# Performance work log

Measured on AMD Instinct MI355X. Metric: run time of the kernel, lower is better.

## Reference

```python
import jax, jax.numpy as jnp
import numpy as np

V, D, DI, S, B, NI = 32000, 1024, 768, 512, 8, 197
EPS = 1e-5

def _ln(x, g, b):
    m = jnp.mean(x, axis=-1, keepdims=True)
    v = jnp.var(x, axis=-1, keepdims=True)
    return (x - m) * jax.lax.rsqrt(v + EPS) * g + b

def _pos_enc(seq_len, d):
    pos = np.arange(seq_len)[:, None].astype(np.float32)
    i = np.arange(0, d, 2).astype(np.float32)
    ang = pos / np.power(10000.0, i / d)
    pe = np.zeros((seq_len, d), dtype=np.float32)
    pe[:, 0::2] = np.sin(ang)
    pe[:, 1::2] = np.cos(ang)
    return jnp.asarray(pe)

def setup_inputs() -> dict:
    key = jax.random.key(0)
    ks = jax.random.split(key, 24)
    def rn(k, shape, scale=0.02):
        return jax.random.normal(k, shape, dtype=jnp.float32) * scale
    return {
        'tokens': jax.random.randint(ks[0], (B, S), 0, V),
        'img_emb': jax.random.normal(ks[1], (B, NI, DI), dtype=jnp.float32),
        'emb_table': rn(ks[2], (V, D), 1.0),
        'Wq1': rn(ks[3], (D, D)), 'bq1': jnp.zeros((D,), jnp.float32),
        'Wk1': rn(ks[4], (D, D)), 'bk1': jnp.zeros((D,), jnp.float32),
        'Wv1': rn(ks[5], (D, D)), 'bv1': jnp.zeros((D,), jnp.float32),
        'g1': jnp.ones((D,), jnp.float32), 'b1': jnp.zeros((D,), jnp.float32),
        'Wq2': rn(ks[6], (D, D)), 'bq2': jnp.zeros((D,), jnp.float32),
        'Wk2': rn(ks[7], (DI, D)), 'bk2': jnp.zeros((D,), jnp.float32),
        'Wv2': rn(ks[8], (DI, D)), 'bv2': jnp.zeros((D,), jnp.float32),
        'g2': jnp.ones((D,), jnp.float32), 'b2': jnp.zeros((D,), jnp.float32),
        'Wp': rn(ks[9], (D, V)), 'bp': jnp.zeros((V,), jnp.float32),
    }

def _forward(tokens, img_emb, emb_table, Wq1, bq1, Wk1, bk1, Wv1, bv1, g1, b1,
             Wq2, bq2, Wk2, bk2, Wv2, bv2, g2, b2, Wp, bp):
    scale = 1.0 / jnp.sqrt(jnp.float32(D))
    x = emb_table[tokens] + _pos_enc(S, D)[None]  # [B,S,D]
    # masked (causal) self-attention
    Q = x @ Wq1 + bq1
    K = x @ Wk1 + bk1
    Vv = x @ Wv1 + bv1
    attn = jnp.einsum('bqd,bkd->bqk', Q, K) * scale
    causal = jnp.tril(jnp.ones((S, S), dtype=bool))
    attn = jnp.where(causal[None], attn, -jnp.inf)
    A = jax.nn.softmax(attn, axis=-1)
    x = _ln(A @ Vv + x, g1, b1)
    # cross-attention over image tokens
    Q2 = x @ Wq2 + bq2
    K2 = img_emb @ Wk2 + bk2
    V2 = img_emb @ Wv2 + bv2
    A2 = jax.nn.softmax(jnp.einsum('bqd,bkd->bqk', Q2, K2) * scale, axis=-1)
    x = _ln(A2 @ V2 + x, g2, b2)
    # vocab projection (note: Decoder.forward never calls self.ff)
    return x @ Wp + bp  # [B,S,V]

def reference(tokens, img_emb, emb_table, Wq1, bq1, Wk1, bk1, Wv1, bv1, g1, b1,
              Wq2, bq2, Wk2, bk2, Wv2, bv2, g2, b2, Wp, bp):
    return _forward(tokens, img_emb, emb_table, Wq1, bq1, Wk1, bk1, Wv1, bv1, g1, b1,
                    Wq2, bq2, Wk2, bk2, Wv2, bv2, g2, b2, Wp, bp)
```

## Files before the change

kernel.cpp:

```cpp
#include <hip/hip_runtime.h>
#include <hip/hip_bf16.h>


#define DEV __device__ __forceinline__

typedef __bf16 bf16x8 __attribute__((ext_vector_type(8)));
typedef float f32x4 __attribute__((ext_vector_type(4)));
typedef unsigned int u32;
typedef __hip_bfloat16 bf16;

DEV void llds16(const void* g, void* l) {
  __builtin_amdgcn_global_load_lds((const __attribute__((address_space(1))) u32*)g,
                                   (__attribute__((address_space(3))) u32*)l, 16, 0, 0);
}

DEV float wredsum(float v){
#pragma unroll
  for (int o = 32; o; o >>= 1) v += __shfl_xor(v, o, 64);
  return v;
}
DEV float wredmax(float v){
#pragma unroll
  for (int o = 32; o; o >>= 1) v = fmaxf(v, __shfl_xor(v, o, 64));
  return v;
}

DEV void store_out(float* p, float v){ *p = v; }
DEV void store_out(bf16* p, float v){ *p = __float2bfloat16(v); }

template<typename OutT>
__global__ __launch_bounds__(512, 1) void gemm256_kernel(
    const bf16* __restrict__ A, const bf16* __restrict__ Bt, OutT* __restrict__ C,
    const float* __restrict__ bias, int M, int N, int K, int lda, int ldb, int ldc)
{
  __shared__ alignas(16) char lds[131072];
  const int tid  = threadIdx.x;
  const int wave = tid >> 6, lane = tid & 63;
  const int lo = lane & 15, hi = lane >> 4;
  const int hi2 = hi ^ ((lo >> 1) & 3);
  const int wr = wave >> 2, wc = wave & 3;
  const int koff = (((lane & 3) ^ ((lane >> 3) & 3)) << 3);

  const int nbx = M >> 8;
  const int nwg = nbx * (N >> 8);
  int id = blockIdx.x;
  int g = (nwg & 7) ? id : ((id & 7) * (nwg >> 3) + (id >> 3));
  const int row0 = (g % nbx) * 256, col0 = (g / nbx) * 256;
  const int NT = K >> 5;
  const int srow = lane >> 2;

  auto stageA = [&](int t) {
    char* base = lds + (t & 3) * 32768;
    const int kk = (t << 5) + koff;
#pragma unroll
    for (int j = 0; j < 2; j++) {
      const int seg = j * 8 + wave;
      llds16(A + (long)(row0 + seg * 16 + srow) * lda + kk, base + seg * 1024);
    }
  };
  auto stageB = [&](int t) {
    char* base = lds + (t & 3) * 32768 + 16384;
    const int kk = (t << 5) + koff;
#pragma unroll
    for (int j = 0; j < 2; j++) {
      const int seg = j * 8 + wave;
      llds16(Bt + (long)(col0 + seg * 16 + srow) * ldb + kk, base + seg * 1024);
    }
  };

  f32x4 acc[8][4] = {};

  stageA(0); stageB(0);
  stageA(1); stageB(1);
  stageA(2); stageB(2);
  asm volatile("s_waitcnt vmcnt(8)" ::: "memory");
  __builtin_amdgcn_s_barrier();
  asm volatile("" ::: "memory");

  for (int t = 0; t < NT; t++) {
    char* As = lds + (t & 3) * 32768;
    char* Bs = As + 16384;
    bf16x8 af[4], bfv[4];
#pragma unroll
    for (int m = 0; m < 4; m++)
      af[m] = *(const bf16x8*)(As + ((wr * 128 + m * 16 + lo) << 6) + (hi2 << 4));
#pragma unroll
    for (int n = 0; n < 4; n++)
      bfv[n] = *(const bf16x8*)(Bs + ((wc * 64 + n * 16 + lo) << 6) + (hi2 << 4));
    if (t + 3 < NT) stageA(t + 3);
    __builtin_amdgcn_s_setprio(1);
#pragma unroll
    for (int m = 0; m < 4; m++)
#pragma unroll
      for (int n = 0; n < 4; n++)
        acc[m][n] = __builtin_amdgcn_mfma_f32_16x16x32_bf16(af[m], bfv[n], acc[m][n], 0, 0, 0);
    __builtin_amdgcn_s_setprio(0);
    asm volatile("" ::: "memory");
    __builtin_amdgcn_s_barrier();
    asm volatile("" ::: "memory");
#pragma unroll
    for (int m = 0; m < 4; m++)
      af[m] = *(const bf16x8*)(As + ((wr * 128 + (m + 4) * 16 + lo) << 6) + (hi2 << 4));
    if (t + 3 < NT) stageB(t + 3);
    __builtin_amdgcn_s_setprio(1);
#pragma unroll
    for (int m = 0; m < 4; m++)
#pragma unroll
      for (int n = 0; n < 4; n++)
        acc[m + 4][n] = __builtin_amdgcn_mfma_f32_16x16x32_bf16(af[m], bfv[n], acc[m + 4][n], 0, 0, 0);
    __builtin_amdgcn_s_setprio(0);
    if (t < NT - 3)       asm volatile("s_waitcnt vmcnt(8)" ::: "memory");
    else if (t == NT - 3) asm volatile("s_waitcnt vmcnt(4)" ::: "memory");
    else                  asm volatile("s_waitcnt vmcnt(0)" ::: "memory");
    __builtin_amdgcn_s_barrier();
    asm volatile("" ::: "memory");
  }

#pragma unroll
  for (int m = 0; m < 8; m++) {
    const int r = row0 + wr * 128 + m * 16 + hi * 4;
#pragma unroll
    for (int n = 0; n < 4; n++) {
      const int c = col0 + wc * 64 + n * 16 + lo;
      const float bb = bias ? bias[c] : 0.0f;
#pragma unroll
      for (int j = 0; j < 4; j++)
        store_out(&C[(long)(r + j) * ldc + c], acc[m][n][j] + bb);
    }
  }
}

template<typename OutT>
__global__ __launch_bounds__(256) void gemm_bt_kernel(
    const bf16* __restrict__ A, const bf16* __restrict__ Bt, OutT* __restrict__ C,
    const float* __restrict__ bias, int M, int N, int K,
    int lda, int ldb, int ldc, long sA, long sB, long sC)
{
  A  += (long)blockIdx.z * sA;
  Bt += (long)blockIdx.z * sB;
  C  += (long)blockIdx.z * sC;
  __shared__ alignas(16) char lds[32768];
  const int tid = threadIdx.x;
  const int wave = tid >> 6, lane = tid & 63;
  const int lo = lane & 15, hi = lane >> 4;
  const int hi2 = hi ^ ((lo >> 1) & 3);
  const int wr = wave >> 1, wc = wave & 1;
  const int row0 = blockIdx.x * 128, col0 = blockIdx.y * 128;
  const int srow  = lane >> 2;
  const int skoff = (((lane & 3) ^ ((lane >> 3) & 3)) << 3);
  const int NT = K >> 5;

  auto stage = [&](int t) {
    char* base = lds + (t & 1) * 16384;
    const int kk = (t << 5) + skoff;
#pragma unroll
    for (int c = 0; c < 2; ++c) {
      const int seg = c*4 + wave;
      int ra = row0 + seg*16 + srow; ra = ra < M ? ra : M-1;
      llds16(A + (long)ra*lda + kk, base + seg*1024);
      int rb = col0 + seg*16 + srow; rb = rb < N ? rb : N-1;
      llds16(Bt + (long)rb*ldb + kk, base + 8192 + seg*1024);
    }
  };

  f32x4 acc[4][4] = {};

  stage(0);
  asm volatile("s_waitcnt vmcnt(0)" ::: "memory");
  __builtin_amdgcn_s_barrier();
  __builtin_amdgcn_sched_barrier(0);

  for (int t = 0; t < NT; t++) {
    const char* As = lds + (t & 1) * 16384;
    const char* Bs = As + 8192;
    if (t + 1 < NT) stage(t + 1);
    bf16x8 af[4], bfv[4];
#pragma unroll
    for (int m = 0; m < 4; m++)
      af[m] = *(const bf16x8*)(As + ((wr*64 + m*16 + lo) << 6) + (hi2 << 4));
#pragma unroll
    for (int n = 0; n < 4; n++)
      bfv[n] = *(const bf16x8*)(Bs + ((wc*64 + n*16 + lo) << 6) + (hi2 << 4));
    __builtin_amdgcn_s_setprio(1);
#pragma unroll
    for (int m = 0; m < 4; m++)
#pragma unroll
      for (int n = 0; n < 4; n++)
        acc[m][n] = __builtin_amdgcn_mfma_f32_16x16x32_bf16(af[m], bfv[n], acc[m][n], 0, 0, 0);
    __builtin_amdgcn_s_setprio(0);
    __builtin_amdgcn_sched_barrier(0);
    asm volatile("s_waitcnt vmcnt(0)" ::: "memory");
    __builtin_amdgcn_sched_barrier(0);
    __builtin_amdgcn_s_barrier();
    __builtin_amdgcn_sched_barrier(0);
  }

#pragma unroll
  for (int m = 0; m < 4; m++) {
    const int rbase = row0 + wr*64 + m*16 + hi*4;
#pragma unroll
    for (int n = 0; n < 4; n++) {
      const int cc = col0 + wc*64 + n*16 + lo;
      if (cc >= N) continue;
      const float bb = bias ? bias[cc] : 0.0f;
#pragma unroll
      for (int j = 0; j < 4; j++) {
        const int rr = rbase + j;
        if (rr < M) store_out(&C[(long)rr*ldc + cc], acc[m][n][j] + bb);
      }
    }
  }
}

__global__ __launch_bounds__(256) void wprep4_kernel(
    const float* W0, const float* W1, const float* W2, const float* W3,
    bf16* T0, bf16* T1, bf16* T2, bf16* T3, int K, int N)
{
  const int z = blockIdx.z;
  const float* W = z == 0 ? W0 : z == 1 ? W1 : z == 2 ? W2 : W3;
  bf16* T = z == 0 ? T0 : z == 1 ? T1 : z == 2 ? T2 : T3;
  __shared__ bf16 t[32][33];
  const int k0 = blockIdx.x * 32, n0 = blockIdx.y * 32;
  const int tx = threadIdx.x & 31, ty = threadIdx.x >> 5;
#pragma unroll
  for (int i = 0; i < 4; i++)
    t[ty + i*8][tx] = __float2bfloat16(W[(long)(k0 + ty + i*8)*N + n0 + tx]);
  __syncthreads();
#pragma unroll
  for (int i = 0; i < 4; i++)
    T[(long)(n0 + ty + i*8)*K + k0 + tx] = t[tx][ty + i*8];
}

__global__ __launch_bounds__(256) void transpose_pad_kernel(
    const bf16* __restrict__ in, bf16* __restrict__ out,
    int R, int Cc, int inLD, int outLD, long inBatch, long outBatch)
{
  in  += (long)blockIdx.z * inBatch;
  out += (long)blockIdx.z * outBatch;
  __shared__ bf16 t[32][33];
  const int r0 = blockIdx.x * 32, c0 = blockIdx.y * 32;
  const int tx = threadIdx.x & 31, ty = threadIdx.x >> 5;
#pragma unroll
  for (int i = 0; i < 4; i++) {
    const int r = r0 + ty + i*8;
    bf16 v = __float2bfloat16(0.0f);
    if (r < R) v = in[(long)r*inLD + c0 + tx];
    t[ty + i*8][tx] = v;
  }
  __syncthreads();
#pragma unroll
  for (int i = 0; i < 4; i++) {
    const int oc = r0 + tx;
    const int orow = c0 + ty + i*8;
    if (oc < outLD) out[(long)orow*outLD + oc] = t[tx][ty + i*8];
  }
}

__global__ __launch_bounds__(256) void concat_bias_kernel(
    const float* a, const float* b, const float* c, int n1, int n2, int n3, float* out)
{
  const int i = blockIdx.x * 256 + threadIdx.x;
  if (i >= n1 + n2 + n3) return;
  out[i] = i < n1 ? a[i] : (i < n1 + n2 ? b[i - n1] : c[i - n1 - n2]);
}

__global__ __launch_bounds__(256) void embed_kernel(
    const int* __restrict__ tok, const float* __restrict__ tbl,
    float* __restrict__ xf, bf16* __restrict__ xb)
{
  const int row = blockIdx.x;
  const int s = row & 511;
  const float pos = (float)s;
  const float* te = tbl + (long)tok[row] * 1024;
  const int d0 = threadIdx.x * 4;
  float4 v = *(const float4*)(te + d0);
  float o[4] = {v.x, v.y, v.z, v.w};
#pragma unroll
  for (int k = 0; k < 4; k++) {
    const int d = d0 + k;
    const int i2 = d & ~1;
    const float ang = pos * exp2f((float)i2 * -0.0129762816f);
    o[k] += (d & 1) ? __cosf(ang) : __sinf(ang);
  }
  *(float4*)(xf + (long)row*1024 + d0) = make_float4(o[0], o[1], o[2], o[3]);
#pragma unroll
  for (int k = 0; k < 4; k++) xb[(long)row*1024 + d0 + k] = __float2bfloat16(o[k]);
}

__global__ __launch_bounds__(256) void cvt_bf16_kernel(const float* __restrict__ in, bf16* __restrict__ out, long n)
{
  long i = (long)blockIdx.x * blockDim.x + threadIdx.x;
  if (i < n) out[i] = __float2bfloat16(in[i]);
}

__global__ __launch_bounds__(64) void softmax_causal_kernel(
    const float* __restrict__ Sc, bf16* __restrict__ P)
{
  const int row = blockIdx.x;
  const int q = row & 511;
  const float* srow = Sc + (long)row * 512;
  bf16* prow = P + (long)row * 512;
  const int lane = threadIdx.x;
  const float scale = 0.03125f;
  float mx = -1e30f;
  for (int j = lane; j <= q; j += 64) mx = fmaxf(mx, srow[j]);
  mx = wredmax(mx);
  float sum = 0.0f;
  for (int j = lane; j <= q; j += 64) sum += expf((srow[j] - mx) * scale);
  sum = wredsum(sum);
  const float inv = 1.0f / sum;
  for (int j = lane; j < 512; j += 64) {
    float p = (j <= q) ? expf((srow[j] - mx) * scale) * inv : 0.0f;
    prow[j] = __float2bfloat16(p);
  }
}

__global__ __launch_bounds__(64) void softmax_cross_kernel(
    const float* __restrict__ Sc, bf16* __restrict__ P)
{
  const int row = blockIdx.x;
  const float* srow = Sc + (long)row * 224;
  bf16* prow = P + (long)row * 224;
  const int lane = threadIdx.x;
  const float scale = 0.03125f;
  float mx = -1e30f;
  for (int j = lane; j < 197; j += 64) mx = fmaxf(mx, srow[j]);
  mx = wredmax(mx);
  float sum = 0.0f;
  for (int j = lane; j < 197; j += 64) sum += expf((srow[j] - mx) * scale);
  sum = wredsum(sum);
  const float inv = 1.0f / sum;
  for (int j = lane; j < 224; j += 64) {
    float p = (j < 197) ? expf((srow[j] - mx) * scale) * inv : 0.0f;
    prow[j] = __float2bfloat16(p);
  }
}

__global__ __launch_bounds__(256) void add_ln_kernel(
    const float* __restrict__ Acc, const float* __restrict__ Res,
    const float* __restrict__ g, const float* __restrict__ b,
    float* __restrict__ outf, bf16* __restrict__ outb)
{
  const int row = blockIdx.x;
  const float* a = Acc + (long)row * 1024;
  const float* r = Res + (long)row * 1024;
  float vals[4], s = 0.0f, ss = 0.0f;
#pragma unroll
  for (int i = 0; i < 4; i++) {
    const int d = threadIdx.x + i*256;
    const float v = a[d] + r[d];
    vals[i] = v; s += v; ss += v*v;
  }
  s = wredsum(s); ss = wredsum(ss);
  __shared__ float sh[8];
  const int wave = threadIdx.x >> 6, lane = threadIdx.x & 63;
  if (lane == 0) { sh[wave] = s; sh[wave+4] = ss; }
  __syncthreads();
  s  = sh[0] + sh[1] + sh[2] + sh[3];
  ss = sh[4] + sh[5] + sh[6] + sh[7];
  const float mean = s * (1.0f/1024.0f);
  const float var  = ss * (1.0f/1024.0f) - mean*mean;
  const float inv  = rsqrtf(var + 1e-5f);
#pragma unroll
  for (int i = 0; i < 4; i++) {
    const int d = threadIdx.x + i*256;
    const float y = (vals[i] - mean) * inv * g[d] + b[d];
    if (outf) outf[(long)row*1024 + d] = y;
    outb[(long)row*1024 + d] = __float2bfloat16(y);
  }
}

extern "C" void kernel_launch(void* const* d_in, const int* in_sizes, int n_in,
                              void* d_out, int out_size, void* d_ws, size_t ws_size,
                              hipStream_t stream) {
  const int*   tokens = (const int*)  d_in[0];
  const float* img    = (const float*)d_in[1];
  const float* emb    = (const float*)d_in[2];
  const float* Wq1    = (const float*)d_in[3];
  const float* bq1    = (const float*)d_in[4];
  const float* Wk1    = (const float*)d_in[5];
  const float* bk1    = (const float*)d_in[6];
  const float* Wv1    = (const float*)d_in[7];
  const float* bv1    = (const float*)d_in[8];
  const float* g1     = (const float*)d_in[9];
  const float* b1     = (const float*)d_in[10];
  const float* Wq2    = (const float*)d_in[11];
  const float* bq2    = (const float*)d_in[12];
  const float* Wk2    = (const float*)d_in[13];
  const float* bk2    = (const float*)d_in[14];
  const float* Wv2    = (const float*)d_in[15];
  const float* bv2    = (const float*)d_in[16];
  const float* g2     = (const float*)d_in[17];
  const float* b2     = (const float*)d_in[18];
  const float* Wp     = (const float*)d_in[19];
  const float* bp     = (const float*)d_in[20];
  float* out = (float*)d_out;

  const int B = 8, S = 512, D = 1024, DI = 768, NI = 197, NIP = 224, V = 32000;
  const int M = B * S;
  const int MI = B * NI;

  char* ws = (char*)d_ws;
  size_t off = 0;
  auto alloc = [&](size_t bytes) -> char* {
    char* p = ws + off; off += (bytes + 255) & ~(size_t)255; return p;
  };
  bf16* Wq1t = (bf16*)alloc((size_t)D*D*2);
  bf16* Wk1t = (bf16*)alloc((size_t)D*D*2);
  bf16* Wv1t = (bf16*)alloc((size_t)D*D*2);
  bf16* Wq2t = (bf16*)alloc((size_t)D*D*2);
  bf16* Wk2t = (bf16*)alloc((size_t)D*DI*2);
  bf16* Wv2t = (bf16*)alloc((size_t)D*DI*2);
  bf16* Wpt  = (bf16*)alloc((size_t)V*D*2);
  float* bqkv= (float*)alloc((size_t)3*D*4);
  float* bkv2= (float*)alloc((size_t)2*D*4);
  float* xf  = (float*)alloc((size_t)M*D*4);
  bf16*  xb  = (bf16*) alloc((size_t)M*D*2);
  bf16*  imgb= (bf16*) alloc((size_t)MI*DI*2);
  bf16*  QKV = (bf16*) alloc((size_t)M*3*D*2);
  bf16*  Vt  = (bf16*) alloc((size_t)M*D*2);
  float* sc1 = (float*)alloc((size_t)B*S*S*4);
  bf16*  P1  = (bf16*) alloc((size_t)B*S*S*2);
  float* ao1 = (float*)alloc((size_t)M*D*4);
  float* x2f = (float*)alloc((size_t)M*D*4);
  bf16*  x2b = (bf16*) alloc((size_t)M*D*2);
  bf16*  Q2  = (bf16*) alloc((size_t)M*D*2);
  bf16*  KV2 = (bf16*) alloc((size_t)MI*2*D*2);
  bf16*  V2t = (bf16*) alloc((size_t)B*D*NIP*2);
  float* sc2 = (float*)alloc((size_t)B*S*NIP*4);
  bf16*  P2  = (bf16*) alloc((size_t)B*S*NIP*2);
  float* ao2 = (float*)alloc((size_t)M*D*4);
  bf16*  x3b = (bf16*) alloc((size_t)M*D*2);
  (void)ws_size; (void)in_sizes; (void)n_in; (void)out_size;

  wprep4_kernel<<<dim3(D/32,  D/32, 4), 256, 0, stream>>>(Wq1, Wk1, Wv1, Wq2, Wq1t, Wk1t, Wv1t, Wq2t, D, D);
  wprep4_kernel<<<dim3(DI/32, D/32, 2), 256, 0, stream>>>(Wk2, Wv2, nullptr, nullptr, Wk2t, Wv2t, nullptr, nullptr, DI, D);
  wprep4_kernel<<<dim3(D/32,  V/32, 1), 256, 0, stream>>>(Wp, nullptr, nullptr, nullptr, Wpt, nullptr, nullptr, nullptr, D, V);
  concat_bias_kernel<<<(3*D+255)/256, 256, 0, stream>>>(bq1, bk1, bv1, D, D, D, bqkv);
  concat_bias_kernel<<<(2*D+255)/256, 256, 0, stream>>>(bk2, bv2, nullptr, D, D, 0, bkv2);

  embed_kernel<<<M, 256, 0, stream>>>(tokens, emb, xf, xb);
  {
    long n = (long)MI * DI;
    cvt_bf16_kernel<<<(int)((n + 255)/256), 256, 0, stream>>>(img, imgb, n);
  }

  auto gemmF = [&](const bf16* A, const bf16* Bt, float* C, const float* bias,
                   int m, int n, int k, int lda, int ldb, int ldc,
                   long sA, long sB, long sC, int batch) {
    dim3 g((m+127)/128, (n+127)/128, batch);
    gemm_bt_kernel<float><<<g, 256, 0, stream>>>(A, Bt, C, bias, m, n, k, lda, ldb, ldc, sA, sB, sC);
  };
  auto gemmB = [&](const bf16* A, const bf16* Bt, bf16* C, const float* bias,
                   int m, int n, int k, int lda, int ldb, int ldc,
                   long sA, long sB, long sC, int batch) {
    dim3 g((m+127)/128, (n+127)/128, batch);
    gemm_bt_kernel<bf16><<<g, 256, 0, stream>>>(A, Bt, C, bias, m, n, k, lda, ldb, ldc, sA, sB, sC);
  };

  gemm256_kernel<bf16><<<dim3((M/256)*(3*D/256)), 512, 0, stream>>>(
      xb, Wq1t, QKV, bqkv, M, 3*D, D, D, D, 3*D);
  transpose_pad_kernel<<<dim3(S/32, D/32, B), 256, 0, stream>>>(
      QKV + 2*D, Vt, S, D, 3*D, S, (long)S*3*D, (long)D*S);
  gemmF(QKV, QKV + D, sc1, nullptr, S, S, D, 3*D, 3*D, S, (long)S*3*D, (long)S*3*D, (long)S*S, B);
  softmax_causal_kernel<<<M, 64, 0, stream>>>(sc1, P1);
  gemmF(P1, Vt, ao1, nullptr, S, D, S, S, S, D, (long)S*S, (long)D*S, (long)S*D, B);
  add_ln_kernel<<<M, 256, 0, stream>>>(ao1, xf, g1, b1, x2f, x2b);

  gemm256_kernel<bf16><<<dim3((M/256)*(D/256)), 512, 0, stream>>>(
      x2b, Wq2t, Q2, bq2, M, D, D, D, D, D);
  gemmB(imgb, Wk2t, KV2, bkv2, MI, 2*D, DI, DI, DI, 2*D, 0, 0, 0, 1);
  transpose_pad_kernel<<<dim3((NIP+31)/32, D/32, B), 256, 0, stream>>>(
      KV2 + D, V2t, NI, D, 2*D, NIP, (long)NI*2*D, (long)D*NIP);
  gemmF(Q2, KV2, sc2, nullptr, S, NI, D, D, 2*D, NIP, (long)S*D, (long)NI*2*D, (long)S*NIP, B);
  softmax_cross_kernel<<<M, 64, 0, stream>>>(sc2, P2);
  gemmF(P2, V2t, ao2, nullptr, S, D, NIP, NIP, NIP, D, (long)S*NIP, (long)D*NIP, (long)S*D, B);
  add_ln_kernel<<<M, 256, 0, stream>>>(ao2, x2f, g2, b2, nullptr, x3b);

  gemm256_kernel<float><<<dim3((M/256)*(V/256)), 512, 0, stream>>>(
      x3b, Wpt, out, bp, M, V, D, D, D, V);
}
```

Before: 669.9 us.

## Skip masked causal tiles and keep residual activations in bf16

The QK^T GEMM now launches only lower-triangular 128x128 tiles (10 per batch) and maps block index to tile coordinates, and the PV GEMM truncates its K loop at the causal boundary. Intermediate attention outputs and residual streams are stored as bf16 instead of fp32, removing the fp32 copies of x and x2 and vectorising the embed and add+LN stores. This cuts FLOPs and memory traffic in the attention stages. The risks are extra rounding in the residual path, and the upper tiles of sc1 are left unwritten, which is harmless only if the softmax never reads masked scores.

Measured after the change: 655.8 us. 2.1% less time.

```diff
diff --git a/kernel.cpp b/kernel.cpp
--- a/kernel.cpp
+++ b/kernel.cpp
@@ -24,6 +24,8 @@
   for (int o = 32; o; o >>= 1) v = fmaxf(v, __shfl_xor(v, o, 64));
   return v;
 }
+
+DEV float b2f(unsigned short x){ return __uint_as_float((u32)x << 16); }
 
 DEV void store_out(float* p, float v){ *p = v; }
 DEV void store_out(bf16* p, float v){ *p = __float2bfloat16(v); }
@@ -134,21 +136,24 @@
 __global__ __launch_bounds__(256) void gemm_bt_kernel(
     const bf16* __restrict__ A, const bf16* __restrict__ Bt, OutT* __restrict__ C,
     const float* __restrict__ bias, int M, int N, int K,
-    int lda, int ldb, int ldc, long sA, long sB, long sC)
+    int lda, int ldb, int ldc, long sA, long sB, long sC, int tri, int kcausal)
 {
   A  += (long)blockIdx.z * sA;
   Bt += (long)blockIdx.z * sB;
   C  += (long)blockIdx.z * sC;
   __shared__ alignas(16) char lds[32768];
+  int bx = blockIdx.x, by = blockIdx.y;
+  if (tri) { int t = blockIdx.x, i = 0; while (t > i) { t -= i + 1; i++; } bx = i; by = t; }
   const int tid = threadIdx.x;
   const int wave = tid >> 6, lane = tid & 63;
   const int lo = lane & 15, hi = lane >> 4;
   const int hi2 = hi ^ ((lo >> 1) & 3);
   const int wr = wave >> 1, wc = wave & 1;
-  const int row0 = blockIdx.x * 128, col0 = blockIdx.y * 128;
+  const int row0 = bx * 128, col0 = by * 128;
   const int srow  = lane >> 2;
   const int skoff = (((lane & 3) ^ ((lane >> 3) & 3)) << 3);
-  const int NT = K >> 5;
+  const int Keff = kcausal ? (K < row0 + 128 ? K : row0 + 128) : K;
+  const int NT = Keff >> 5;
 
   auto stage = [&](int t) {
     char* base = lds + (t & 1) * 16384;
@@ -266,7 +271,7 @@
 
 __global__ __launch_bounds__(256) void embed_kernel(
     const int* __restrict__ tok, const float* __restrict__ tbl,
-    float* __restrict__ xf, bf16* __restrict__ xb)
+    bf16* __restrict__ xb)
 {
   const int row = blockIdx.x;
   const int s = row & 511;
@@ -282,9 +287,10 @@
     const float ang = pos * exp2f((float)i2 * -0.0129762816f);
     o[k] += (d & 1) ? __cosf(ang) : __sinf(ang);
   }
-  *(float4*)(xf + (long)row*1024 + d0) = make_float4(o[0], o[1], o[2], o[3]);
-#pragma unroll
-  for (int k = 0; k < 4; k++) xb[(long)row*1024 + d0 + k] = __float2bfloat16(o[k]);
+  bf16 ob[4];
+#pragma unroll
+  for (int k = 0; k < 4; k++) ob[k] = __float2bfloat16(o[k]);
+  *(ushort4*)((unsigned short*)xb + (long)row*1024 + d0) = *(ushort4*)ob;
 }
 
 __global__ __launch_bounds__(256) void cvt_bf16_kernel(const float* __restrict__ in, bf16* __restrict__ out, long n)
@@ -337,20 +343,20 @@
 }
 
 __global__ __launch_bounds__(256) void add_ln_kernel(
-    const float* __restrict__ Acc, const float* __restrict__ Res,
+    const bf16* __restrict__ Acc, const bf16* __restrict__ Res,
     const float* __restrict__ g, const float* __restrict__ b,
-    float* __restrict__ outf, bf16* __restrict__ outb)
+    bf16* __restrict__ outb)
 {
   const int row = blockIdx.x;
-  const float* a = Acc + (long)row * 1024;
-  const float* r = Res + (long)row * 1024;
-  float vals[4], s = 0.0f, ss = 0.0f;
-#pragma unroll
-  for (int i = 0; i < 4; i++) {
-    const int d = threadIdx.x + i*256;
-    const float v = a[d] + r[d];
-    vals[i] = v; s += v; ss += v*v;
-  }
+  const unsigned short* a = (const unsigned short*)Acc + (long)row * 1024;
+  const unsigned short* r = (const unsigned short*)Res + (long)row * 1024;
+  const int d0 = threadIdx.x * 4;
+  ushort4 av = *(const ushort4*)(a + d0);
+  ushort4 rv = *(const ushort4*)(r + d0);
+  float vals[4] = { b2f(av.x) + b2f(rv.x), b2f(av.y) + b2f(rv.y),
+                    b2f(av.z) + b2f(rv.z), b2f(av.w) + b2f(rv.w) };
+  float s = vals[0] + vals[1] + vals[2] + vals[3];
+  float ss = vals[0]*vals[0] + vals[1]*vals[1] + vals[2]*vals[2] + vals[3]*vals[3];
   s = wredsum(s); ss = wredsum(ss);
   __shared__ float sh[8];
   const int wave = threadIdx.x >> 6, lane = threadIdx.x & 63;
@@ -361,13 +367,13 @@
   const float mean = s * (1.0f/1024.0f);
   const float var  = ss * (1.0f/1024.0f) - mean*mean;
   const float inv  = rsqrtf(var + 1e-5f);
+  bf16 ob[4];
 #pragma unroll
   for (int i = 0; i < 4; i++) {
-    const int d = threadIdx.x + i*256;
-    const float y = (vals[i] - mean) * inv * g[d] + b[d];
-    if (outf) outf[(long)row*1024 + d] = y;
-    outb[(long)row*1024 + d] = __float2bfloat16(y);
-  }
+    const int d = d0 + i;
+    ob[i] = __float2bfloat16((vals[i] - mean) * inv * g[d] + b[d]);
+  }
+  *(ushort4*)((unsigned short*)outb + (long)row*1024 + d0) = *(ushort4*)ob;
 }
 
 extern "C" void kernel_launch(void* const* d_in, const int* in_sizes, int n_in,
@@ -414,22 +420,20 @@
   bf16* Wpt  = (bf16*)alloc((size_t)V*D*2);
   float* bqkv= (float*)alloc((size_t)3*D*4);
   float* bkv2= (float*)alloc((size_t)2*D*4);
-  float* xf  = (float*)alloc((size_t)M*D*4);
   bf16*  xb  = (bf16*) alloc((size_t)M*D*2);
   bf16*  imgb= (bf16*) alloc((size_t)MI*DI*2);
   bf16*  QKV = (bf16*) alloc((size_t)M*3*D*2);
   bf16*  Vt  = (bf16*) alloc((size_t)M*D*2);
   float* sc1 = (float*)alloc((size_t)B*S*S*4);
   bf16*  P1  = (bf16*) alloc((size_t)B*S*S*2);
-  float* ao1 = (float*)alloc((size_t)M*D*4);
-  float* x2f = (float*)alloc((size_t)M*D*4);
+  bf16*  ao1 = (bf16*) alloc((size_t)M*D*2);
   bf16*  x2b = (bf16*) alloc((size_t)M*D*2);
   bf16*  Q2  = (bf16*) alloc((size_t)M*D*2);
   bf16*  KV2 = (bf16*) alloc((size_t)MI*2*D*2);
   bf16*  V2t = (bf16*) alloc((size_t)B*D*NIP*2);
   float* sc2 = (float*)alloc((size_t)B*S*NIP*4);
   bf16*  P2  = (bf16*) alloc((size_t)B*S*NIP*2);
-  float* ao2 = (float*)alloc((size_t)M*D*4);
+  bf16*  ao2 = (bf16*) alloc((size_t)M*D*2);
   bf16*  x3b = (bf16*) alloc((size_t)M*D*2);
   (void)ws_size; (void)in_sizes; (void)n_in; (void)out_size;
 
@@ -439,7 +443,7 @@
   concat_bias_kernel<<<(3*D+255)/256, 256, 0, stream>>>(bq1, bk1, bv1, D, D, D, bqkv);
   concat_bias_kernel<<<(2*D+255)/256, 256, 0, stream>>>(bk2, bv2, nullptr, D, D, 0, bkv2);
 
-  embed_kernel<<<M, 256, 0, stream>>>(tokens, emb, xf, xb);
+  embed_kernel<<<M, 256, 0, stream>>>(tokens, emb, xb);
   {
     long n = (long)MI * DI;
     cvt_bf16_kernel<<<(int)((n + 255)/256), 256, 0, stream>>>(img, imgb, n);
@@ -449,23 +453,27 @@
                    int m, int n, int k, int lda, int ldb, int ldc,
                    long sA, long sB, long sC, int batch) {
     dim3 g((m+127)/128, (n+127)/128, batch);
-    gemm_bt_kernel<float><<<g, 256, 0, stream>>>(A, Bt, C, bias, m, n, k, lda, ldb, ldc, sA, sB, sC);
+    gemm_bt_kernel<float><<<g, 256, 0, stream>>>(A, Bt, C, bias, m, n, k, lda, ldb, ldc, sA, sB, sC, 0, 0);
   };
   auto gemmB = [&](const bf16* A, const bf16* Bt, bf16* C, const float* bias,
                    int m, int n, int k, int lda, int ldb, int ldc,
                    long sA, long sB, long sC, int batch) {
     dim3 g((m+127)/128, (n+127)/128, batch);
-    gemm_bt_kernel<bf16><<<g, 256, 0, stream>>>(A, Bt, C, bias, m, n, k, lda, ldb, ldc, sA, sB, sC);
+    gemm_bt_kernel<bf16><<<g, 256, 0, stream>>>(A, Bt, C, bias, m, n, k, lda, ldb, ldc, sA, sB, sC, 0, 0);
   };
 
   gemm256_kernel<bf16><<<dim3((M/256)*(3*D/256)), 512, 0, stream>>>(
       xb, Wq1t, QKV, bqkv, M, 3*D, D, D, D, 3*D);
   transpose_pad_kernel<<<dim3(S/32, D/32, B), 256, 0, stream>>>(
       QKV + 2*D, Vt, S, D, 3*D, S, (long)S*3*D, (long)D*S);
-  gemmF(QKV, QKV + D, sc1, nullptr, S, S, D, 3*D, 3*D, S, (long)S*3*D, (long)S*3*D, (long)S*S, B);
+  gemm_bt_kernel<float><<<dim3(10, 1, B), 256, 0, stream>>>(
+      QKV, QKV + D, sc1, nullptr, S, S, D, 3*D, 3*D, S,
+      (long)S*3*D, (long)S*3*D, (long)S*S, 1, 0);
   softmax_causal_kernel<<<M, 64, 0, stream>>>(sc1, P1);
-  gemmF(P1, Vt, ao1, nullptr, S, D, S, S, S, D, (long)S*S, (long)D*S, (long)S*D, B);
-  add_ln_kernel<<<M, 256, 0, stream>>>(ao1, xf, g1, b1, x2f, x2b);
+  gemm_bt_kernel<bf16><<<dim3(S/128, D/128, B), 256, 0, stream>>>(
+      P1, Vt, ao1, nullptr, S, D, S, S, S, D,
+      (long)S*S, (long)D*S, (long)S*D, 0, 1);
+  add_ln_kernel<<<M, 256, 0, stream>>>(ao1, xb, g1, b1, x2b);
 
   gemm256_kernel<bf16><<<dim3((M/256)*(D/256)), 512, 0, stream>>>(
       x2b, Wq2t, Q2, bq2, M, D, D, D, D, D);
@@ -474,8 +482,8 @@
       KV2 + D, V2t, NI, D, 2*D, NIP, (long)NI*2*D, (long)D*NIP);
   gemmF(Q2, KV2, sc2, nullptr, S, NI, D, D, 2*D, NIP, (long)S*D, (long)NI*2*D, (long)S*NIP, B);
   softmax_cross_kernel<<<M, 64, 0, stream>>>(sc2, P2);
-  gemmF(P2, V2t, ao2, nullptr, S, D, NIP, NIP, NIP, D, (long)S*NIP, (long)D*NIP, (long)S*D, B);
-  add_ln_kernel<<<M, 256, 0, stream>>>(ao2, x2f, g2, b2, nullptr, x3b);
+  gemmB(P2, V2t, ao2, nullptr, S, D, NIP, NIP, NIP, D, (long)S*NIP, (long)D*NIP, (long)S*D, B);
+  add_ln_kernel<<<M, 256, 0, stream>>>(ao2, x2b, g2, b2, x3b);
 
   gemm256_kernel<float><<<dim3((M/256)*(V/256)), 512, 0, stream>>>(
       x3b, Wpt, out, bp, M, V, D, D, D, V);
```
